# Kernel tuning notes

Measured on AMD Instinct MI355X. Metric: run time of the kernel, lower is better.

## Reference

```python
import jax, jax.numpy as jnp
import numpy as np
import math

B, L, E, H, NL, M, S, R = 4, 1024, 512, 8, 2, 2048, 256, 2
Dh = E // H
NEG = jnp.finfo(jnp.float32).min


def _posenc(n, d):
    pos = np.arange(n)[:, None].astype(np.float32)
    div = np.exp(np.arange(0, d, 2).astype(np.float32) * (-math.log(10000.0) / d))
    pe = np.zeros((n, d), np.float32)
    pe[:, 0::2] = np.sin(pos * div)
    pe[:, 1::2] = np.cos(pos * div)
    return jnp.asarray(pe)


def _temb(t, dim, max_positions=10000):
    half = dim // 2
    freqs = jnp.exp(jnp.arange(half, dtype=jnp.float32) * (-math.log(max_positions) / (half - 1)))
    a = t[:, None] * freqs[None, :]
    return jnp.concatenate([jnp.sin(a), jnp.cos(a)], axis=1)


def _ln(x, s, b, eps=1e-5):
    m = x.mean(-1, keepdims=True)
    v = jnp.mean((x - m) ** 2, axis=-1, keepdims=True)
    return (x - m) * jax.lax.rsqrt(v + eps) * s + b


def _gelu(x):
    return jax.nn.gelu(x, approximate=False)


def _block(h, W, b, lns, lnb, mW1, mb1, mW2, mb2, mask):
    # prenorm self-attention
    z = _ln(h, lns[0], lnb[0])
    q = (z @ W[0] + b[0]).reshape(B, L, H, Dh) / math.sqrt(Dh)
    k = (z @ W[1] + b[1]).reshape(B, L, H, Dh)
    v = (z @ W[2] + b[2]).reshape(B, L, H, Dh)
    logits = jnp.einsum('bqhd,bkhd->bhqk', q, k)
    att = jax.nn.softmax(jnp.where(mask, logits, NEG), axis=-1)
    o = jnp.einsum('bhqk,bkhd->bqhd', att, v).reshape(B, L, E)
    h = h + o @ W[3] + b[3]
    # prenorm feed-forward
    z = _ln(h, lns[1], lnb[1])
    return h + _gelu(z @ mW1 + mb1) @ mW2 + mb2


def setup_inputs():
    key = jax.random.key(0)
    ks = iter(jax.random.split(key, 48))
    def nrm(shape, s=0.02):
        return jax.random.normal(next(ks), shape, jnp.float32) * s
    inp = {
        'x': jax.random.randint(next(ks), (B, L), 0, S),
        't': jax.random.uniform(next(ks), (B,), jnp.float32) * 1000.0,
        'embed': nrm((S, E), 1.0),
        'attn_W': nrm((2, NL, 4, E, E)),
        'attn_b': jnp.zeros((2, NL, 4, E)),
        'ln_s': jnp.ones((2, NL, 2, E)),
        'ln_b': jnp.zeros((2, NL, 2, E)),
        'mlp_W1': nrm((2, NL, E, M)),
        'mlp_b1': jnp.zeros((2, NL, M)),
        'mlp_W2': nrm((2, NL, M, E)),
        'mlp_b2': jnp.zeros((2, NL, E)),
        'ca_Wq': nrm((E, E)),
        'ca_Wk': nrm((E, E)), 'ca_bk': jnp.zeros((E,)),
        'ca_Wv': nrm((E, E)), 'ca_bv': jnp.zeros((E,)),
        'ca_Wo': nrm((E, E)), 'ca_bo': jnp.zeros((E,)),
        'ro_ln1_s': jnp.ones((E,)), 'ro_ln1_b': jnp.zeros((E,)),
        'ro_ln2_s': jnp.ones((E,)), 'ro_ln2_b': jnp.zeros((E,)),
        'in_W': nrm((E, 2 * E)), 'in_b': jnp.zeros((2 * E,)),
        'tmlp_W1': nrm((E, M)), 'tmlp_b1': jnp.zeros((M,)),
        'tmlp_W2': nrm((M, 4 * E)), 'tmlp_b2': jnp.zeros((4 * E,)),
        'res_W1': nrm((R, 2 * E, M)), 'res_b1': jnp.zeros((R, M)),
        'res_W2': nrm((R, M, 2 * E)), 'res_b2': jnp.zeros((R, 2 * E)),
        'res_ln_s': jnp.ones((R, 2 * E)), 'res_ln_b': jnp.zeros((R, 2 * E)),
        'film_W': nrm((R, 4 * E, 4 * E)), 'film_b': jnp.ones((R, 4 * E)),
        'out_W': nrm((2 * E, S)), 'out_b': jnp.zeros((S,)),
    }
    return inp


def reference(x, t, embed, attn_W, attn_b, ln_s, ln_b, mlp_W1, mlp_b1, mlp_W2, mlp_b2,
              ca_Wq, ca_Wk, ca_bk, ca_Wv, ca_bv, ca_Wo, ca_bo,
              ro_ln1_s, ro_ln1_b, ro_ln2_s, ro_ln2_b,
              in_W, in_b, tmlp_W1, tmlp_b1, tmlp_W2, tmlp_b2,
              res_W1, res_b1, res_W2, res_b2, res_ln_s, res_ln_b,
              film_W, film_b, out_W, out_b):
    temb = _temb(t, E)                       # [B,E]
    tok = embed[x]                           # [B,L,E]
    pe = _posenc(L, E)[None]
    cond = temb[:, None, :]
    il = jnp.arange(L)
    causal = (il[None, :] <= il[:, None])[None, None]  # [1,1,L,L]
    embeds = []
    for d in range(2):
        if d == 0:  # l2r: shift right, prepend temb token, causal mask
            h = jnp.concatenate([cond, tok[:, :-1]], axis=1)
            mask = causal
        else:       # r2l: shift left, append temb token, anti-causal mask
            h = jnp.concatenate([tok[:, 1:], cond], axis=1)
            mask = jnp.swapaxes(causal, -1, -2)
        h = h + pe
        for l in range(NL):
            h = _block(h, attn_W[d, l], attn_b[d, l], ln_s[d, l], ln_b[d, l],
                       mlp_W1[d, l], mlp_b1[d, l], mlp_W2[d, l], mlp_b2[d, l], mask)
        embeds.append(h)
    l2r_embed, r2l_embed = embeds
    # AttentionReadout (prenorm) with joint-mask cross-attention
    inputs = l2r_embed + r2l_embed
    l2r_n = _ln(l2r_embed, ro_ln1_s, ro_ln1_b)
    r2l_n = _ln(r2l_embed, ro_ln2_s, ro_ln2_b)
    q = ((l2r_n + r2l_n) @ ca_Wq).reshape(B, L, H, Dh) / math.sqrt(Dh)
    allv = jnp.concatenate([temb[:, None], l2r_n, r2l_n], axis=1)  # [B,2L+1,E]
    k = (allv @ ca_Wk + ca_bk).reshape(B, 2 * L + 1, H, Dh)
    v = (allv @ ca_Wv + ca_bv).reshape(B, 2 * L + 1, H, Dh)
    logits = jnp.einsum('bqhd,bkhd->bhqk', q, k)  # [B,H,L,2L+1]
    m_l2r = il[None, :] > il[:, None]   # triu, diag=1
    m_r2l = il[None, :] < il[:, None]   # tril, diag=-1
    joint = jnp.concatenate([jnp.ones((L, 1), bool), m_l2r, m_r2l], axis=-1)[None, None]
    att = jax.nn.softmax(jnp.where(joint, logits, NEG), axis=-1)
    xat = jnp.einsum('bhqk,bkhd->bqhd', att, v).reshape(B, L, E)
    xat = xat @ ca_Wo + ca_bo + inputs
    # ResidualReadout: FiLM-conditioned residual MLP stack
    t4 = _gelu(temb @ tmlp_W1 + tmlp_b1) @ tmlp_W2 + tmlp_b2  # [B,4E]
    h = xat @ in_W + in_b                                     # [B,L,2E]
    for i in range(R):
        film = t4 @ film_W[i] + film_b[i]
        z = _gelu(h @ res_W1[i] + res_b1[i]) @ res_W2[i] + res_b2[i]
        h = _ln(h + z, res_ln_s[i], res_ln_b[i])
        fa, fb = jnp.split(film[:, None, :], 2, axis=-1)
        h = fa * h + fb
    return h @ out_W + out_b  # [B,L,S]
```

## Files before the change

### kernel.cpp

```cpp
#include <hip/hip_runtime.h>
#include <hip/hip_bf16.h>


#define NEGF -3.4028235e38f
#define LOG2E 1.4426950408889634f

using bf16x8 = __attribute__((ext_vector_type(8))) short;
using f32x4  = __attribute__((ext_vector_type(4))) float;

__device__ inline float bf2f(unsigned short u) {
    return __uint_as_float(((unsigned int)u) << 16);
}
__device__ inline unsigned short f2b(float f) {
    unsigned int u = __float_as_uint(f);
    return (unsigned short)((u + 0x7fff + ((u >> 16) & 1)) >> 16);
}

__device__ inline void gl_lds16(const void* g, void* l) {
    __builtin_amdgcn_global_load_lds(
        (const __attribute__((address_space(1))) void*)(uintptr_t)g,
        (__attribute__((address_space(3))) void*)(unsigned int)(uintptr_t)l,
        16, 0, 0);
}

template<int BM>
__global__ __launch_bounds__(256) void gemm_bf16_k(
    const unsigned short* __restrict__ A,
    const unsigned short* __restrict__ Wt0, const unsigned short* __restrict__ Wt1,
    const float* __restrict__ bias0, const float* __restrict__ bias1, int mhalf,
    const float* __restrict__ res,
    float* __restrict__ Cf, unsigned short* __restrict__ Cb,
    unsigned short* __restrict__ CbK, unsigned short* __restrict__ Ct, int ldkv,
    int M, int N, int K, float alpha, int gelu_flag, int qkv)
{
    constexpr int MF  = BM / 32;
    constexpr int NAC = BM * 4 / 256;
    __shared__ unsigned short As[3][BM * 32];
    __shared__ unsigned short Bs[3][4096];
    const int tid  = threadIdx.x;
    const int wid  = tid >> 6;
    const int lane = tid & 63;
    const int wy   = wid >> 1, wx = wid & 1;
    const int koff = lane >> 4, l16 = lane & 15;

    const int flat = blockIdx.y * gridDim.x + blockIdx.x;
    const int cpx  = (gridDim.x * gridDim.y) >> 3;
    const int swz  = (flat & 7) * cpx + (flat >> 3);
    const int m0 = (swz / gridDim.x) * BM, n0 = (swz % gridDim.x) * 128;

    const unsigned short* Wt = (m0 < mhalf) ? Wt0 : Wt1;
    const float* bias = (m0 < mhalf) ? bias0 : bias1;

    const unsigned short* aG[NAC];
    const unsigned short* bG[2];
    #pragma unroll
    for (int i = 0; i < NAC; ++i) {
        int c = tid + i * 256;
        int r = ((c >> 6) << 4) | (c & 15), kk = ((c >> 4) & 3) << 3;
        aG[i] = A + (size_t)(m0 + r) * K + kk;
    }
    #pragma unroll
    for (int i = 0; i < 2; ++i) {
        int c = tid + i * 256;
        int r = ((c >> 6) << 4) | (c & 15), kk = ((c >> 4) & 3) << 3;
        bG[i] = Wt + (size_t)(n0 + r) * K + kk;
    }

    f32x4 acc[MF][4] = {};
    const int nk = K >> 5;

    auto stage = [&](int buf, int k0) {
        #pragma unroll
        for (int i = 0; i < NAC; ++i)
            gl_lds16(aG[i] + k0, &As[buf][(size_t)(i * 256 + wid * 64) * 8]);
        #pragma unroll
        for (int i = 0; i < 2; ++i)
            gl_lds16(bG[i] + k0, &Bs[buf][(size_t)(i * 256 + wid * 64) * 8]);
    };

    stage(0, 0);
    if (nk > 1) stage(1, 32);
    int cur = 0, nxt = 2;
    for (int it = 0; it < nk; ++it) {
        const int ahead = nk - 1 - it;
        if (ahead >= 2) stage(nxt, (it + 2) << 5);
        if constexpr (BM == 128) {
            if (ahead >= 2)      asm volatile("s_waitcnt vmcnt(8)" ::: "memory");
            else if (ahead == 1) asm volatile("s_waitcnt vmcnt(4)" ::: "memory");
            else                 asm volatile("s_waitcnt vmcnt(0)" ::: "memory");
        } else {
            if (ahead >= 2)      asm volatile("s_waitcnt vmcnt(6)" ::: "memory");
            else if (ahead == 1) asm volatile("s_waitcnt vmcnt(3)" ::: "memory");
            else                 asm volatile("s_waitcnt vmcnt(0)" ::: "memory");
        }
        __builtin_amdgcn_s_barrier();

        bf16x8 af[MF], bfr[4];
        const int foff = (koff * 16 + l16) * 8;
        #pragma unroll
        for (int i = 0; i < MF; ++i)
            af[i] = *(const bf16x8*)&As[cur][(size_t)((wy * MF + i) * 64) * 8 + foff];
        #pragma unroll
        for (int j = 0; j < 4; ++j)
            bfr[j] = *(const bf16x8*)&Bs[cur][(size_t)((wx * 4 + j) * 64) * 8 + foff];
        #pragma unroll
        for (int i = 0; i < MF; ++i)
            #pragma unroll
            for (int j = 0; j < 4; ++j)
                acc[i][j] = __builtin_amdgcn_mfma_f32_16x16x32_bf16(
                    af[i], bfr[j], acc[i][j], 0, 0, 0);

        cur = (cur == 2) ? 0 : cur + 1;
        nxt = (nxt == 2) ? 0 : nxt + 1;
    }

    #pragma unroll
    for (int i = 0; i < MF; ++i) {
        const int rbase = m0 + wy * (MF * 16) + i * 16 + koff * 4;
        #pragma unroll
        for (int j = 0; j < 4; ++j) {
            const int gn = n0 + wx * 64 + j * 16 + l16;
            const float bs = bias ? bias[gn] : 0.f;
            if (qkv) {
                const int seg = gn >> 9, gnl = gn & 511;
                const float av = (seg == 0) ? 0.125f : 1.0f;
                unsigned short o[4];
                #pragma unroll
                for (int r = 0; r < 4; ++r) o[r] = f2b((acc[i][j][r] + bs) * av);
                if (seg == 0) {
                    #pragma unroll
                    for (int r = 0; r < 4; ++r)
                        Cb[(size_t)(rbase + r) * 512 + gnl] = o[r];
                } else if (seg == 1) {
                    #pragma unroll
                    for (int r = 0; r < 4; ++r)
                        CbK[(size_t)(rbase + r) * 512 + gnl] = o[r];
                } else {
                    const int hh = gnl >> 6, dh = gnl & 63;
                    const int bb = rbase >> 10, l0 = rbase & 1023;
                    *(ushort4*)(Ct + ((size_t)(bb * 8 + hh) * 64 + dh) * 1024 + l0) =
                        make_ushort4(o[0], o[1], o[2], o[3]);
                }
            } else {
                float vr[4];
                #pragma unroll
                for (int r = 0; r < 4; ++r) {
                    float v = (acc[i][j][r] + bs) * alpha;
                    if (gelu_flag) v = 0.5f * v * (1.0f + erff(v * 0.70710678118654752f));
                    const size_t idx = (size_t)(rbase + r) * N + gn;
                    if (res) v += res[idx];
                    if (Cf) Cf[idx] = v;
                    if (Cb) Cb[idx] = f2b(v);
                    vr[r] = v;
                }
                if (Ct) {
                    const int hh = gn >> 6, dh = gn & 63;
                    const int bb = rbase / ldkv;
                    const int l0 = rbase - bb * ldkv;
                    *(ushort4*)(Ct + ((size_t)(bb * 8 + hh) * 64 + dh) * ldkv + l0) =
                        make_ushort4(f2b(vr[0]), f2b(vr[1]), f2b(vr[2]), f2b(vr[3]));
                }
            }
        }
    }
}

__global__ __launch_bounds__(256) void wconv(
    const float* __restrict__ src, unsigned short* __restrict__ dst,
    int K, int N, long sstride, long dstride)
{
    __shared__ float t[64][65];
    const int n0 = blockIdx.x * 64, k0 = blockIdx.y * 64;
    const float* s = src + (size_t)blockIdx.z * sstride;
    unsigned short* d = dst + (size_t)blockIdx.z * dstride;
    const int tid = threadIdx.x;
    #pragma unroll
    for (int i = 0; i < 4; ++i) {
        int lin = i * 1024 + tid * 4;
        int r = lin >> 6, c = lin & 63;
        float4 v = *(const float4*)(s + (size_t)(k0 + r) * N + n0 + c);
        t[r][c] = v.x; t[r][c + 1] = v.y; t[r][c + 2] = v.z; t[r][c + 3] = v.w;
    }
    __syncthreads();
    #pragma unroll
    for (int i = 0; i < 8; ++i) {
        int lin = i * 512 + tid * 2;
        int rn = lin >> 6, ck = lin & 63;
        ushort2 o;
        o.x = f2b(t[ck][rn]); o.y = f2b(t[ck + 1][rn]);
        *(ushort2*)(d + (size_t)(n0 + rn) * K + k0 + ck) = o;
    }
}

__global__ __launch_bounds__(256) void skinny_k(
    const float* __restrict__ A, const float* __restrict__ W,
    float* __restrict__ P, int N, int K)
{
    const int n = blockIdx.x * 256 + threadIdx.x;
    const int s = blockIdx.y;
    const int k0 = s * 32;
    float a0 = 0.f, a1 = 0.f, a2 = 0.f, a3 = 0.f;
    #pragma unroll 8
    for (int k = k0; k < k0 + 32; ++k) {
        float w = W[(size_t)k * N + n];
        a0 = fmaf(A[k], w, a0);
        a1 = fmaf(A[K + k], w, a1);
        a2 = fmaf(A[2 * K + k], w, a2);
        a3 = fmaf(A[3 * K + k], w, a3);
    }
    float* p = P + (size_t)s * 4 * N;
    p[n] = a0; p[N + n] = a1; p[2 * N + n] = a2; p[3 * N + n] = a3;
}

__global__ __launch_bounds__(256) void skinny_red(
    const float* __restrict__ P, const float* __restrict__ bias,
    float* __restrict__ C, int N, int nsplit, int gelu_flag)
{
    const int n = blockIdx.x * 256 + threadIdx.x;
    const int r = blockIdx.y;
    float acc = 0.f;
    for (int s = 0; s < nsplit; ++s) acc += P[((size_t)s * 4 + r) * N + n];
    float v = acc + (bias ? bias[n] : 0.f);
    if (gelu_flag) v = 0.5f * v * (1.0f + erff(v * 0.70710678118654752f));
    C[(size_t)r * N + n] = v;
}

__global__ __launch_bounds__(256) void ln_kernel(
    const float* __restrict__ X, const float* __restrict__ X2,
    const float* __restrict__ s, const float* __restrict__ b,
    float* __restrict__ Yf, unsigned short* __restrict__ Yb,
    int D, const float* __restrict__ film, int rows_per_batch, long pstride)
{
    const int row = blockIdx.x;
    const int tid = threadIdx.x;
    const float* x = X + (size_t)row * D;
    const float* x2 = X2 ? X2 + (size_t)row * D : nullptr;
    const float* se = s + (size_t)(row >> 12) * pstride;
    const float* be = b + (size_t)(row >> 12) * pstride;

    float sum = 0.f, sq = 0.f;
    for (int c = tid * 2; c < D; c += 512) {
        float2 v2 = *(const float2*)(x + c);
        if (x2) { float2 w2 = *(const float2*)(x2 + c); v2.x += w2.x; v2.y += w2.y; }
        sum += v2.x + v2.y;
        sq  += v2.x * v2.x + v2.y * v2.y;
    }
    __shared__ float r1[4], r2[4];
    __shared__ float s_mean, s_rstd;
    for (int off = 32; off > 0; off >>= 1) {
        sum += __shfl_down(sum, off);
        sq  += __shfl_down(sq,  off);
    }
    if ((tid & 63) == 0) { r1[tid >> 6] = sum; r2[tid >> 6] = sq; }
    __syncthreads();
    if (tid == 0) {
        float ts = r1[0] + r1[1] + r1[2] + r1[3];
        float tq = r2[0] + r2[1] + r2[2] + r2[3];
        float mean = ts / (float)D;
        float var = tq / (float)D - mean * mean;
        s_mean = mean;
        s_rstd = rsqrtf(var + 1e-5f);
    }
    __syncthreads();
    const float mean = s_mean, rstd = s_rstd;
    const float* fa = nullptr; const float* fb = nullptr;
    if (film) {
        int batch = row / rows_per_batch;
        fa = film + (size_t)batch * 2 * D;
        fb = fa + D;
    }
    for (int c = tid * 2; c < D; c += 512) {
        float2 v2 = *(const float2*)(x + c);
        if (x2) { float2 w2 = *(const float2*)(x2 + c); v2.x += w2.x; v2.y += w2.y; }
        float y0 = (v2.x - mean) * rstd * se[c] + be[c];
        float y1 = (v2.y - mean) * rstd * se[c + 1] + be[c + 1];
        if (film) { y0 = fa[c] * y0 + fb[c]; y1 = fa[c + 1] * y1 + fb[c + 1]; }
        if (Yf) *(float2*)(Yf + (size_t)row * D + c) = make_float2(y0, y1);
        if (Yb) *(ushort2*)(Yb + (size_t)row * D + c) = make_ushort2(f2b(y0), f2b(y1));
    }
}

__global__ __launch_bounds__(256) void readout_fuse(
    const float* __restrict__ L2R, const float* __restrict__ R2L,
    const float* __restrict__ s1, const float* __restrict__ b1,
    const float* __restrict__ s2, const float* __restrict__ b2,
    const unsigned short* __restrict__ tembb,
    float* __restrict__ Z, unsigned short* __restrict__ allv,
    unsigned short* __restrict__ SUM)
{
    const int row = blockIdx.x;
    const int tid = threadIdx.x;
    if (row >= 4096) {
        const int b = row - 4096;
        if (tid < 64)
            ((uint4*)(allv + (size_t)b * 2080 * 512))[tid] =
                ((const uint4*)(tembb + b * 512))[tid];
        return;
    }
    const int b = row >> 10, i = row & 1023;
    const float* x1 = L2R + (size_t)row * 512;
    const float* x2 = R2L + (size_t)row * 512;
    const int c = tid * 2;
    float2 a1 = *(const float2*)(x1 + c);
    float2 a2 = *(const float2*)(x2 + c);

    float su1 = a1.x + a1.y, sk1 = a1.x * a1.x + a1.y * a1.y;
    float su2 = a2.x + a2.y, sk2 = a2.x * a2.x + a2.y * a2.y;
    __shared__ float rr[4][4];
    __shared__ float st[4];
    for (int off = 32; off > 0; off >>= 1) {
        su1 += __shfl_down(su1, off);
        sk1 += __shfl_down(sk1, off);
        su2 += __shfl_down(su2, off);
        sk2 += __shfl_down(sk2, off);
    }
    if ((tid & 63) == 0) {
        rr[tid >> 6][0] = su1; rr[tid >> 6][1] = sk1;
        rr[tid >> 6][2] = su2; rr[tid >> 6][3] = sk2;
    }
    __syncthreads();
    if (tid == 0) {
        float t0 = rr[0][0] + rr[1][0] + rr[2][0] + rr[3][0];
        float t1 = rr[0][1] + rr[1][1] + rr[2][1] + rr[3][1];
        float t2 = rr[0][2] + rr[1][2] + rr[2][2] + rr[3][2];
        float t3 = rr[0][3] + rr[1][3] + rr[2][3] + rr[3][3];
        float m1 = t0 / 512.f, m2 = t2 / 512.f;
        st[0] = m1;
        st[1] = rsqrtf(t1 / 512.f - m1 * m1 + 1e-5f);
        st[2] = m2;
        st[3] = rsqrtf(t3 / 512.f - m2 * m2 + 1e-5f);
    }
    __syncthreads();
    const float m1 = st[0], r1v = st[1], m2 = st[2], r2v = st[3];

    *(float2*)(Z + (size_t)row * 512 + c) = make_float2(a1.x + a2.x, a1.y + a2.y);

    float n1x = (a1.x - m1) * r1v * s1[c]     + b1[c];
    float n1y = (a1.y - m1) * r1v * s1[c + 1] + b1[c + 1];
    float n2x = (a2.x - m2) * r2v * s2[c]     + b2[c];
    float n2y = (a2.y - m2) * r2v * s2[c + 1] + b2[c + 1];

    unsigned short* l2rn = allv + ((size_t)(b * 2080 + 1 + i)) * 512;
    unsigned short* r2ln = allv + ((size_t)(b * 2080 + 1025 + i)) * 512;
    *(ushort2*)(l2rn + c) = make_ushort2(f2b(n1x), f2b(n1y));
    *(ushort2*)(r2ln + c) = make_ushort2(f2b(n2x), f2b(n2y));
    *(ushort2*)(SUM + (size_t)row * 512 + c) =
        make_ushort2(f2b(n1x + n2x), f2b(n1y + n2y));
}

__global__ void temb_kernel(const float* __restrict__ t, float* __restrict__ temb,
                            unsigned short* __restrict__ tembb)
{
    int b = blockIdx.x;
    int i = threadIdx.x;
    float f = expf((float)i * (-9.210340371976184f / 255.0f));
    float a = t[b] * f;
    float sv = sinf(a), cv = cosf(a);
    temb[b * 512 + i]        = sv;
    temb[b * 512 + 256 + i]  = cv;
    tembb[b * 512 + i]       = f2b(sv);
    tembb[b * 512 + 256 + i] = f2b(cv);
}

__global__ void embed_kernel(const int* __restrict__ x, const float* __restrict__ temb,
                             const float* __restrict__ embed,
                             float* __restrict__ l2r, float* __restrict__ r2l)
{
    const int i = blockIdx.x;
    const int b = blockIdx.y;
    const int d = blockIdx.z;
    float* out = (d == 0 ? l2r : r2l) + ((size_t)(b * 1024 + i) * 512);
    const float* src;
    if (d == 0) src = (i == 0)    ? temb + b * 512 : embed + (size_t)x[b * 1024 + (i - 1)] * 512;
    else        src = (i == 1023) ? temb + b * 512 : embed + (size_t)x[b * 1024 + (i + 1)] * 512;
    for (int e = threadIdx.x; e < 512; e += 256) {
        int j = e >> 1;
        float div = expf((float)(2 * j) * (-9.210340371976184f / 512.0f));
        float ang = (float)i * div;
        float pe = (e & 1) ? cosf(ang) : sinf(ang);
        out[e] = src[e] + pe;
    }
}

__global__ __launch_bounds__(256) void attn_mfma(
    const unsigned short* __restrict__ Q, const unsigned short* __restrict__ K,
    const unsigned short* __restrict__ Vt, unsigned short* __restrict__ O, int mode)
{
    const int E = 512;
    const int LKP = (mode == 2) ? 2080 : 1024;
    const int idf = blockIdx.x;
    const int chunk = gridDim.x >> 3;
    const int w = (idf & 7) * chunk + (idf >> 3);
    int h, bb, dir, qn, qtA;
    if (mode == 2) { qn = 1; qtA = w & 15; h = (w >> 4) & 7; bb = w >> 7; dir = 2; }
    else           { qn = 2; qtA = w & 7;  h = (w >> 3) & 7; bb = w >> 6; dir = bb >> 2; }
    const int tid = threadIdx.x;
    const int wid = tid >> 6, lane = tid & 63;
    const int fr = lane & 15;
    const int fs = lane >> 4;

    __shared__ unsigned short Qs[4096];
    __shared__ unsigned short Ks[4096];
    __shared__ unsigned short Vs[4096];
    __shared__ unsigned short Ps[4][16][72];

    const unsigned short* Kb0 = K + ((size_t)bb * LKP) * E + h * 64;
    const unsigned short* Vb0 = Vt + (size_t)(bb * 8 + h) * 64 * LKP;
    const int sr = tid & 63, sc = tid >> 6;

    uint4 kr0, kr1, vr0, vr1;
#define LOAD_TILE(KT) do {                                                     \
        const unsigned short* Kbase_ = Kb0 + (size_t)((KT) * 64) * E;          \
        const unsigned short* Vbase_ = Vb0 + (KT) * 64;                        \
        kr0 = *(const uint4*)(Kbase_ + (size_t)sr * E + sc * 8);               \
        kr1 = *(const uint4*)(Kbase_ + (size_t)sr * E + (sc + 4) * 8);         \
        vr0 = *(const uint4*)(Vbase_ + (size_t)sr * LKP + sc * 8);             \
        vr1 = *(const uint4*)(Vbase_ + (size_t)sr * LKP + (sc + 4) * 8);       \
    } while (0)

    for (int p = 0; p < qn; ++p) {
        const int qt = (p == 0) ? qtA : (15 - qtA);
        const int q0 = qt * 64;
        const int wq0 = q0 + wid * 16;

        {
            const unsigned short* Qbase = Q + ((size_t)bb * 1024 + q0) * E + h * 64;
            #pragma unroll
            for (int it = 0; it < 2; ++it) {
                int i = tid + it * 256;
                int r = i & 63, c = i >> 6;
                *(uint4*)&Qs[(size_t)(c * 64 + r) * 8] =
                    *(const uint4*)(Qbase + (size_t)r * E + c * 8);
            }
        }
        __syncthreads();
        const bf16x8 aq0 = *(const bf16x8*)&Qs[(size_t)(fs * 64 + wid * 16 + fr) * 8];
        const bf16x8 aq1 = *(const bf16x8*)&Qs[(size_t)((fs + 4) * 64 + wid * 16 + fr) * 8];

        float m_r[4], l_r[4];
        f32x4 o_acc[4] = {};
        #pragma unroll
        for (int r = 0; r < 4; ++r) { m_r[r] = NEGF; l_r[r] = 0.f; }

        int nt, ktA = 1;
        if (dir == 0)      nt = qt + 1;
        else if (dir == 1) nt = 16 - qt;
        else { ktA = (qt >= 1) ? qt : 1; nt = 1 + (qt + 16 - ktA + 1); }
        auto kt_of = [&](int j) -> int {
            if (dir == 0) return j;
            if (dir == 1) return qt + j;
            return (j == 0) ? 0 : (ktA + j - 1);
        };

        LOAD_TILE(kt_of(0));

        for (int j = 0; j < nt; ++j) {
            const int kt = kt_of(j);
            const int k0 = kt * 64;

            asm volatile("s_waitcnt lgkmcnt(0)" ::: "memory");
            __builtin_amdgcn_s_barrier();

            *(uint4*)&Ks[(size_t)(sc * 64 + sr) * 8]       = kr0;
            *(uint4*)&Ks[(size_t)((sc + 4) * 64 + sr) * 8] = kr1;
            *(uint4*)&Vs[(size_t)(sc * 64 + sr) * 8]       = vr0;
            *(uint4*)&Vs[(size_t)((sc + 4) * 64 + sr) * 8] = vr1;
            if (j + 1 < nt) LOAD_TILE(kt_of(j + 1));
            else if (p + 1 < qn) {
                const int qt2 = 15 - qtA;
                const int kt2 = (dir == 0) ? 0 : ((dir == 1) ? qt2 : 0);
                LOAD_TILE(kt2);
            }

            asm volatile("s_waitcnt lgkmcnt(0)" ::: "memory");
            __builtin_amdgcn_s_barrier();

            f32x4 s[4] = {};
            __builtin_amdgcn_s_setprio(1);
            #pragma unroll
            for (int t = 0; t < 4; ++t) {
                bf16x8 bk0 = *(const bf16x8*)&Ks[(size_t)(fs * 64 + t * 16 + fr) * 8];
                bf16x8 bk1 = *(const bf16x8*)&Ks[(size_t)((fs + 4) * 64 + t * 16 + fr) * 8];
                s[t] = __builtin_amdgcn_mfma_f32_16x16x32_bf16(aq0, bk0, s[t], 0, 0, 0);
                s[t] = __builtin_amdgcn_mfma_f32_16x16x32_bf16(aq1, bk1, s[t], 0, 0, 0);
            }
            __builtin_amdgcn_s_setprio(0);

            bool need_mask;
            if (dir != 2) need_mask = (kt == qt);
            else if (kt >= 1 && kt <= 15) need_mask = !((64 * kt - 1) > (q0 + 63));
            else if (kt >= 17)            need_mask = !((64 * kt + 63 - 1025) < q0);
            else                          need_mask = true;
            if (need_mask) {
                #pragma unroll
                for (int t = 0; t < 4; ++t) {
                    #pragma unroll
                    for (int r = 0; r < 4; ++r) {
                        int q = wq0 + fs * 4 + r;
                        int k = k0 + t * 16 + fr;
                        bool valid;
                        if (dir == 0)      valid = (k <= q);
                        else if (dir == 1) valid = (k >= q);
                        else valid = (k == 0) || (k <= 1024 ? (k - 1) > q : (k - 1025) < q);
                        if (!valid) s[t][r] = NEGF;
                    }
                }
            }

            float c_[4], rs[4];
            #pragma unroll
            for (int r = 0; r < 4; ++r) {
                float v = fmaxf(fmaxf(s[0][r], s[1][r]), fmaxf(s[2][r], s[3][r]));
                v = fmaxf(v, __shfl_xor(v, 1));
                v = fmaxf(v, __shfl_xor(v, 2));
                v = fmaxf(v, __shfl_xor(v, 4));
                v = fmaxf(v, __shfl_xor(v, 8));
                float mnew = fmaxf(m_r[r], v);
                c_[r] = exp2f((m_r[r] - mnew) * LOG2E);
                m_r[r] = mnew;
                rs[r] = 0.f;
            }
            #pragma unroll
            for (int t = 0; t < 4; ++t) {
                #pragma unroll
                for (int r = 0; r < 4; ++r) {
                    float pv = exp2f((s[t][r] - m_r[r]) * LOG2E);
                    s[t][r] = pv;
                    rs[r] += pv;
                }
            }
            #pragma unroll
            for (int r = 0; r < 4; ++r) {
                float v = rs[r];
                v += __shfl_xor(v, 1);
                v += __shfl_xor(v, 2);
                v += __shfl_xor(v, 4);
                v += __shfl_xor(v, 8);
                l_r[r] = l_r[r] * c_[r] + v;
                o_acc[0][r] *= c_[r]; o_acc[1][r] *= c_[r];
                o_acc[2][r] *= c_[r]; o_acc[3][r] *= c_[r];
            }

            #pragma unroll
            for (int t = 0; t < 4; ++t)
                #pragma unroll
                for (int r = 0; r < 4; ++r)
                    Ps[wid][fs * 4 + r][t * 16 + fr] = f2b(s[t][r]);

            bf16x8 pa0 = *(const bf16x8*)&Ps[wid][fr][fs * 8];
            bf16x8 pa1 = *(const bf16x8*)&Ps[wid][fr][fs * 8 + 32];
            __builtin_amdgcn_s_setprio(1);
            #pragma unroll
            for (int t = 0; t < 4; ++t) {
                bf16x8 bv0 = *(const bf16x8*)&Vs[(size_t)(fs * 64 + t * 16 + fr) * 8];
                bf16x8 bv1 = *(const bf16x8*)&Vs[(size_t)((fs + 4) * 64 + t * 16 + fr) * 8];
                o_acc[t] = __builtin_amdgcn_mfma_f32_16x16x32_bf16(pa0, bv0, o_acc[t], 0, 0, 0);
                o_acc[t] = __builtin_amdgcn_mfma_f32_16x16x32_bf16(pa1, bv1, o_acc[t], 0, 0, 0);
            }
            __builtin_amdgcn_s_setprio(0);
        }

        unsigned short* Obase = O + ((size_t)bb * 1024 + q0) * E + h * 64;
        float invl[4];
        #pragma unroll
        for (int r = 0; r < 4; ++r) invl[r] = 1.f / l_r[r];
        #pragma unroll
        for (int t = 0; t < 4; ++t)
            #pragma unroll
            for (int r = 0; r < 4; ++r)
                Obase[(size_t)(wid * 16 + fs * 4 + r) * E + t * 16 + fr] =
                    f2b(o_acc[t][r] * invl[r]);

        if (p + 1 < qn) __syncthreads();
    }
#undef LOAD_TILE
}


static inline void gemmb(hipStream_t st, int BM, const unsigned short* A,
                         const unsigned short* Wt0, const unsigned short* Wt1,
                         const float* bias0, const float* bias1, int mhalf,
                         const float* res, float* Cf, unsigned short* Cb,
                         unsigned short* CbK, unsigned short* Ct, int ldkv,
                         int M, int N, int K, float alpha, int gelu, int qkv)
{
    dim3 g(N / 128, M / BM);
    if (BM == 128)
        gemm_bf16_k<128><<<g, dim3(256), 0, st>>>(A, Wt0, Wt1, bias0, bias1, mhalf,
            res, Cf, Cb, CbK, Ct, ldkv, M, N, K, alpha, gelu, qkv);
    else
        gemm_bf16_k<64><<<g, dim3(256), 0, st>>>(A, Wt0, Wt1, bias0, bias1, mhalf,
            res, Cf, Cb, CbK, Ct, ldkv, M, N, K, alpha, gelu, qkv);
}

static inline void sgemm4(hipStream_t st, const float* A, const float* W,
                          const float* bias, float* C, float* P,
                          int N, int K, int gelu)
{
    const int nsplit = K / 32;
    skinny_k<<<dim3(N / 256, nsplit), 256, 0, st>>>(A, W, P, N, K);
    skinny_red<<<dim3(N / 256, 4), 256, 0, st>>>(P, bias, C, N, nsplit, gelu);
}

extern "C" void kernel_launch(void* const* d_in, const int* in_sizes, int n_in,
                              void* d_out, int out_size, void* d_ws, size_t ws_size,
                              hipStream_t stream)
{
    const int*   x      = (const int*)  d_in[0];
    const float* t      = (const float*)d_in[1];
    const float* embedW = (const float*)d_in[2];
    const float* attn_W = (const float*)d_in[3];
    const float* attn_b = (const float*)d_in[4];
    const float* ln_s   = (const float*)d_in[5];
    const float* ln_b   = (const float*)d_in[6];
    const float* mlp_W1 = (const float*)d_in[7];
    const float* mlp_b1 = (const float*)d_in[8];
    const float* mlp_W2 = (const float*)d_in[9];
    const float* mlp_b2 = (const float*)d_in[10];
    const float* ca_Wq  = (const float*)d_in[11];
    const float* ca_Wk  = (const float*)d_in[12];
    const float* ca_bk  = (const float*)d_in[13];
    const float* ca_Wv  = (const float*)d_in[14];
    const float* ca_bv  = (const float*)d_in[15];
    const float* ca_Wo  = (const float*)d_in[16];
    const float* ca_bo  = (const float*)d_in[17];
    const float* ro1s   = (const float*)d_in[18];
    const float* ro1b   = (const float*)d_in[19];
    const float* ro2s   = (const float*)d_in[20];
    const float* ro2b   = (const float*)d_in[21];
    const float* in_W   = (const float*)d_in[22];
    const float* in_b   = (const float*)d_in[23];
    const float* tm_W1  = (const float*)d_in[24];
    const float* tm_b1  = (const float*)d_in[25];
    const float* tm_W2  = (const float*)d_in[26];
    const float* tm_b2  = (const float*)d_in[27];
    const float* res_W1 = (const float*)d_in[28];
    const float* res_b1 = (const float*)d_in[29];
    const float* res_W2 = (const float*)d_in[30];
    const float* res_b2 = (const float*)d_in[31];
    const float* rls    = (const float*)d_in[32];
    const float* rlb    = (const float*)d_in[33];
    const float* film_W = (const float*)d_in[34];
    const float* film_b = (const float*)d_in[35];
    const float* out_W  = (const float*)d_in[36];
    const float* out_b  = (const float*)d_in[37];
    float* out = (float*)d_out;
    (void)ws_size; (void)in_sizes; (void)n_in; (void)out_size;

    char* base = (char*)d_ws;
    size_t off = 0;
    auto alloc = [&](size_t bytes) -> char* {
        char* p = base + off;
        off = (off + bytes + 255) & ~(size_t)255;
        return p;
    };
    float* TEMB  = (float*)alloc(8192);
    float* TM1   = (float*)alloc(32768);
    float* T4    = (float*)alloc(32768);
    float* FILM  = (float*)alloc(32768);
    unsigned short* TEMBb = (unsigned short*)alloc(4096);
    float* SKP   = (float*)alloc(2097152);

    float* HB  = (float*)alloc(16777216);
    float* L2R = HB;
    float* R2L = HB + 4096 * 512;
    float* Z   = (float*)alloc(8388608);
    float* H2  = (float*)alloc(16777216);
    float* Z2  = (float*)alloc(16777216);

    unsigned short* Zb  = (unsigned short*)alloc(8388608);
    unsigned short* Qb  = (unsigned short*)alloc(8388608);
    unsigned short* Kb  = (unsigned short*)alloc(8388608);
    unsigned short* Vb  = (unsigned short*)alloc(8388608);
    unsigned short* Ob  = (unsigned short*)alloc(8388608);
    unsigned short* H2b = (unsigned short*)alloc(8388608);

    unsigned short* BIG = (unsigned short*)alloc(33554432);
    unsigned short* MIDb  = BIG;
    unsigned short* ALLVb = BIG;
    unsigned short* K2b   = BIG + 4259840;
    unsigned short* V2T   = BIG + 8519680;

    unsigned short* WT = (unsigned short*)alloc(45613056);
    const size_t wt_attn = 0,        wt_mlp1 = 4194304, wt_mlp2 = 8388608;
    const size_t wt_caq = 12582912,  wt_cak = 12845056, wt_cav = 13107200,
                 wt_cao = 13369344,  wt_in  = 13631488;
    const size_t wt_res1 = 14155776, wt_res2 = 18350080, wt_out = 22544384;

    wconv<<<dim3(8, 8, 16), 256, 0, stream>>>(attn_W, WT + wt_attn, 512, 512, 262144, 262144);
    wconv<<<dim3(32, 8, 4), 256, 0, stream>>>(mlp_W1, WT + wt_mlp1, 512, 2048, 1048576, 1048576);
    wconv<<<dim3(8, 32, 4), 256, 0, stream>>>(mlp_W2, WT + wt_mlp2, 2048, 512, 1048576, 1048576);
    wconv<<<dim3(8, 8), 256, 0, stream>>>(ca_Wq, WT + wt_caq, 512, 512, 0, 0);
    wconv<<<dim3(8, 8), 256, 0, stream>>>(ca_Wk, WT + wt_cak, 512, 512, 0, 0);
    wconv<<<dim3(8, 8), 256, 0, stream>>>(ca_Wv, WT + wt_cav, 512, 512, 0, 0);
    wconv<<<dim3(8, 8), 256, 0, stream>>>(ca_Wo, WT + wt_cao, 512, 512, 0, 0);
    wconv<<<dim3(16, 8), 256, 0, stream>>>(in_W, WT + wt_in, 512, 1024, 0, 0);
    wconv<<<dim3(32, 16, 2), 256, 0, stream>>>(res_W1, WT + wt_res1, 1024, 2048, 2097152, 2097152);
    wconv<<<dim3(16, 32, 2), 256, 0, stream>>>(res_W2, WT + wt_res2, 2048, 1024, 2097152, 2097152);
    wconv<<<dim3(4, 16), 256, 0, stream>>>(out_W, WT + wt_out, 1024, 256, 0, 0);

    temb_kernel<<<dim3(4), dim3(256), 0, stream>>>(t, TEMB, TEMBb);
    embed_kernel<<<dim3(1024, 4, 2), dim3(256), 0, stream>>>(x, TEMB, embedW, L2R, R2L);

    for (int l = 0; l < 2; ++l) {
        const size_t d1 = 2 + l;
        ln_kernel<<<8192, 256, 0, stream>>>(HB, nullptr,
            ln_s + (l * 2 + 0) * 512, ln_b + (l * 2 + 0) * 512,
            nullptr, Zb, 512, nullptr, 1024, 2048);
        gemmb(stream, 64, Zb,
              WT + wt_attn + (size_t)l * 1048576, WT + wt_attn + d1 * 1048576,
              attn_b + l * 2048, attn_b + d1 * 2048, 4096,
              nullptr, nullptr, Qb, Kb, Vb, 1024, 8192, 1536, 512, 1.f, 0, 1);
        attn_mfma<<<dim3(512), dim3(256), 0, stream>>>(Qb, Kb, Vb, Ob, -1);
        gemmb(stream, 64, Ob,
              WT + wt_attn + (size_t)(l * 4 + 3) * 262144,
              WT + wt_attn + (d1 * 4 + 3) * 262144,
              attn_b + (l * 4 + 3) * 512, attn_b + (d1 * 4 + 3) * 512, 4096,
              HB, HB, nullptr, nullptr, nullptr, 1, 8192, 512, 512, 1.f, 0, 0);
        ln_kernel<<<8192, 256, 0, stream>>>(HB, nullptr,
            ln_s + (l * 2 + 1) * 512, ln_b + (l * 2 + 1) * 512,
            nullptr, Zb, 512, nullptr, 1024, 2048);
        gemmb(stream, 64, Zb,
              WT + wt_mlp1 + (size_t)l * 1048576, WT + wt_mlp1 + d1 * 1048576,
              mlp_b1 + l * 2048, mlp_b1 + d1 * 2048, 4096,
              nullptr, nullptr, MIDb, nullptr, nullptr, 1, 8192, 2048, 512, 1.f, 1, 0);
        gemmb(stream, 64, MIDb,
              WT + wt_mlp2 + (size_t)l * 1048576, WT + wt_mlp2 + d1 * 1048576,
              mlp_b2 + l * 512, mlp_b2 + d1 * 512, 4096,
              HB, HB, nullptr, nullptr, nullptr, 1, 8192, 512, 2048, 1.f, 0, 0);
    }

    readout_fuse<<<dim3(4100), 256, 0, stream>>>(L2R, R2L, ro1s, ro1b, ro2s, ro2b,
                                                 TEMBb, Z, ALLVb, Vb);
    gemmb(stream, 64, Vb, WT + wt_caq, WT + wt_caq, nullptr, nullptr, 1 << 30,
          nullptr, nullptr, Zb, nullptr, nullptr, 1, 4096, 512, 512, 0.125f, 0, 0);
    gemmb(stream, 64, ALLVb, WT + wt_cak, WT + wt_cak, ca_bk, ca_bk, 1 << 30,
          nullptr, nullptr, K2b, nullptr, nullptr, 1, 8320, 512, 512, 1.f, 0, 0);
    gemmb(stream, 64, ALLVb, WT + wt_cav, WT + wt_cav, ca_bv, ca_bv, 1 << 30,
          nullptr, nullptr, nullptr, nullptr, V2T, 2080, 8320, 512, 512, 1.f, 0, 0);
    attn_mfma<<<dim3(512), dim3(256), 0, stream>>>(Zb, K2b, V2T, Ob, 2);
    gemmb(stream, 64, Ob, WT + wt_cao, WT + wt_cao, ca_bo, ca_bo, 1 << 30,
          Z, nullptr, Qb, nullptr, nullptr, 1, 4096, 512, 512, 1.f, 0, 0);

    sgemm4(stream, TEMB, tm_W1, tm_b1, TM1, SKP, 2048, 512, 1);
    sgemm4(stream, TM1, tm_W2, tm_b2, T4, SKP, 2048, 2048, 0);

    gemmb(stream, 64, Qb, WT + wt_in, WT + wt_in, in_b, in_b, 1 << 30,
          nullptr, H2, H2b, nullptr, nullptr, 1, 4096, 1024, 512, 1.f, 0, 0);
    for (int i = 0; i < 2; ++i) {
        sgemm4(stream, T4, film_W + (size_t)i * 4194304, film_b + i * 2048,
               FILM, SKP, 2048, 2048, 0);
        gemmb(stream, 64, H2b, WT + wt_res1 + (size_t)i * 2097152,
              WT + wt_res1 + (size_t)i * 2097152,
              res_b1 + i * 2048, res_b1 + i * 2048, 1 << 30,
              nullptr, nullptr, MIDb, nullptr, nullptr, 1, 4096, 2048, 1024, 1.f, 1, 0);
        gemmb(stream, 64, MIDb, WT + wt_res2 + (size_t)i * 2097152,
              WT + wt_res2 + (size_t)i * 2097152,
              res_b2 + i * 1024, res_b2 + i * 1024, 1 << 30,
              nullptr, Z2, nullptr, nullptr, nullptr, 1, 4096, 1024, 2048, 1.f, 0, 0);
        ln_kernel<<<4096, 256, 0, stream>>>(H2, Z2, rls + i * 1024, rlb + i * 1024,
                                            H2, H2b, 1024, FILM, 1024, 0);
    }

    gemmb(stream, 64, H2b, WT + wt_out, WT + wt_out, out_b, out_b, 1 << 30,
          nullptr, out, nullptr, nullptr, nullptr, 1, 4096, 256, 1024, 1.f, 0, 0);
}
```

Baseline: 1.047 ms.

## Add 256x256-tile 512-thread bf16 GEMM kernel and use it for large GEMMs

Adds a new GEMM kernel with 256x256 output tiles, 512 threads and a triple-buffered global-to-LDS pipeline. It also adds a swizzled block-to-tile mapping and raises wave priority with s_setprio around the MFMA loop. The kernel replaces the 64-row tile kernel for the transformer QKV, out-proj, MLP and readout GEMMs, aiming for more operand reuse per block and fewer global loads. The epilogue is factored into a shared macro. The trade-off is that shapes with small N now launch only 64–256 blocks, which may leave many of the device's CUs idle.

```diff
diff --git a/kernel.cpp b/kernel.cpp
--- a/kernel.cpp
+++ b/kernel.cpp
@@ -22,6 +22,51 @@
         (__attribute__((address_space(3))) void*)(unsigned int)(uintptr_t)l,
         16, 0, 0);
 }
+
+#define GEMM_EPILOGUE(ACC, RBASE, GN)                                          \
+    do {                                                                       \
+        const float bs = bias ? bias[GN] : 0.f;                                \
+        if (qkv) {                                                             \
+            const int seg = (GN) >> 9, gnl = (GN) & 511;                       \
+            const float av = (seg == 0) ? 0.125f : 1.0f;                       \
+            unsigned short o[4];                                               \
+            _Pragma("unroll")                                                  \
+            for (int r = 0; r < 4; ++r) o[r] = f2b(((ACC)[r] + bs) * av);      \
+            if (seg == 0) {                                                    \
+                _Pragma("unroll")                                              \
+                for (int r = 0; r < 4; ++r)                                    \
+                    Cb[(size_t)((RBASE) + r) * 512 + gnl] = o[r];              \
+            } else if (seg == 1) {                                             \
+                _Pragma("unroll")                                              \
+                for (int r = 0; r < 4; ++r)                                    \
+                    CbK[(size_t)((RBASE) + r) * 512 + gnl] = o[r];             \
+            } else {                                                           \
+                const int hh = gnl >> 6, dh = gnl & 63;                        \
+                const int bbx = (RBASE) >> 10, l0 = (RBASE) & 1023;            \
+                *(ushort4*)(Ct + ((size_t)(bbx * 8 + hh) * 64 + dh) * 1024 + l0) = \
+                    make_ushort4(o[0], o[1], o[2], o[3]);                      \
+            }                                                                  \
+        } else {                                                               \
+            float vr[4];                                                       \
+            _Pragma("unroll")                                                  \
+            for (int r = 0; r < 4; ++r) {                                      \
+                float v = ((ACC)[r] + bs) * alpha;                             \
+                if (gelu_flag) v = 0.5f * v * (1.0f + erff(v * 0.70710678118654752f)); \
+                const size_t idx = (size_t)((RBASE) + r) * N + (GN);           \
+                if (res) v += res[idx];                                        \
+                if (Cf) Cf[idx] = v;                                           \
+                if (Cb) Cb[idx] = f2b(v);                                      \
+                vr[r] = v;                                                     \
+            }                                                                  \
+            if (Ct) {                                                          \
+                const int hh = (GN) >> 6, dh = (GN) & 63;                      \
+                const int bbx = (RBASE) / ldkv;                                \
+                const int l0 = (RBASE) - bbx * ldkv;                           \
+                *(ushort4*)(Ct + ((size_t)(bbx * 8 + hh) * 64 + dh) * ldkv + l0) = \
+                    make_ushort4(f2b(vr[0]), f2b(vr[1]), f2b(vr[2]), f2b(vr[3])); \
+            }                                                                  \
+        }                                                                      \
+    } while (0)
 
 template<int BM>
 __global__ __launch_bounds__(256) void gemm_bf16_k(
@@ -120,47 +165,96 @@
         #pragma unroll
         for (int j = 0; j < 4; ++j) {
             const int gn = n0 + wx * 64 + j * 16 + l16;
-            const float bs = bias ? bias[gn] : 0.f;
-            if (qkv) {
-                const int seg = gn >> 9, gnl = gn & 511;
-                const float av = (seg == 0) ? 0.125f : 1.0f;
-                unsigned short o[4];
-                #pragma unroll
-                for (int r = 0; r < 4; ++r) o[r] = f2b((acc[i][j][r] + bs) * av);
-                if (seg == 0) {
-                    #pragma unroll
-                    for (int r = 0; r < 4; ++r)
-                        Cb[(size_t)(rbase + r) * 512 + gnl] = o[r];
-                } else if (seg == 1) {
-                    #pragma unroll
-                    for (int r = 0; r < 4; ++r)
-                        CbK[(size_t)(rbase + r) * 512 + gnl] = o[r];
-                } else {
-                    const int hh = gnl >> 6, dh = gnl & 63;
-                    const int bb = rbase >> 10, l0 = rbase & 1023;
-                    *(ushort4*)(Ct + ((size_t)(bb * 8 + hh) * 64 + dh) * 1024 + l0) =
-                        make_ushort4(o[0], o[1], o[2], o[3]);
-                }
-            } else {
-                float vr[4];
-                #pragma unroll
-                for (int r = 0; r < 4; ++r) {
-                    float v = (acc[i][j][r] + bs) * alpha;
-                    if (gelu_flag) v = 0.5f * v * (1.0f + erff(v * 0.70710678118654752f));
-                    const size_t idx = (size_t)(rbase + r) * N + gn;
-                    if (res) v += res[idx];
-                    if (Cf) Cf[idx] = v;
-                    if (Cb) Cb[idx] = f2b(v);
-                    vr[r] = v;
-                }
-                if (Ct) {
-                    const int hh = gn >> 6, dh = gn & 63;
-                    const int bb = rbase / ldkv;
-                    const int l0 = rbase - bb * ldkv;
-                    *(ushort4*)(Ct + ((size_t)(bb * 8 + hh) * 64 + dh) * ldkv + l0) =
-                        make_ushort4(f2b(vr[0]), f2b(vr[1]), f2b(vr[2]), f2b(vr[3]));
-                }
-            }
+            GEMM_EPILOGUE(acc[i][j], rbase, gn);
+        }
+    }
+}
+
+__global__ __launch_bounds__(512) void gemm_bf16_256(
+    const unsigned short* __restrict__ A,
+    const unsigned short* __restrict__ Wt0, const unsigned short* __restrict__ Wt1,
+    const float* __restrict__ bias0, const float* __restrict__ bias1, int mhalf,
+    const float* __restrict__ res,
+    float* __restrict__ Cf, unsigned short* __restrict__ Cb,
+    unsigned short* __restrict__ CbK, unsigned short* __restrict__ Ct, int ldkv,
+    int M, int N, int K, float alpha, int gelu_flag, int qkv)
+{
+    __shared__ unsigned short As[3][256 * 32];
+    __shared__ unsigned short Bs[3][256 * 32];
+    const int tid  = threadIdx.x;
+    const int wid  = tid >> 6;
+    const int lane = tid & 63;
+    const int wy   = wid >> 2, wx = wid & 3;
+    const int koff = lane >> 4, l16 = lane & 15;
+
+    const int flat = blockIdx.y * gridDim.x + blockIdx.x;
+    const int cpx  = (gridDim.x * gridDim.y) >> 3;
+    const int swz  = (flat & 7) * cpx + (flat >> 3);
+    const int m0 = (swz / gridDim.x) * 256, n0 = (swz % gridDim.x) * 256;
+
+    const unsigned short* Wt = (m0 < mhalf) ? Wt0 : Wt1;
+    const float* bias = (m0 < mhalf) ? bias0 : bias1;
+
+    const unsigned short* aG[2];
+    const unsigned short* bG[2];
+    #pragma unroll
+    for (int i = 0; i < 2; ++i) {
+        int c = tid + i * 512;
+        int r = ((c >> 6) << 4) | (c & 15), kk = ((c >> 4) & 3) << 3;
+        aG[i] = A + (size_t)(m0 + r) * K + kk;
+        bG[i] = Wt + (size_t)(n0 + r) * K + kk;
+    }
+
+    f32x4 acc[8][4] = {};
+    const int nk = K >> 5;
+
+    auto stage = [&](int buf, int k0) {
+        #pragma unroll
+        for (int i = 0; i < 2; ++i)
+            gl_lds16(aG[i] + k0, &As[buf][(size_t)(i * 512 + wid * 64) * 8]);
+        #pragma unroll
+        for (int i = 0; i < 2; ++i)
+            gl_lds16(bG[i] + k0, &Bs[buf][(size_t)(i * 512 + wid * 64) * 8]);
+    };
+
+    stage(0, 0);
+    if (nk > 1) stage(1, 32);
+    int cur = 0, nxt = 2;
+    for (int it = 0; it < nk; ++it) {
+        const int ahead = nk - 1 - it;
+        if (ahead >= 2) stage(nxt, (it + 2) << 5);
+        if (ahead >= 2)      asm volatile("s_waitcnt vmcnt(8)" ::: "memory");
+        else if (ahead == 1) asm volatile("s_waitcnt vmcnt(4)" ::: "memory");
+        else                 asm volatile("s_waitcnt vmcnt(0)" ::: "memory");
+        __builtin_amdgcn_s_barrier();
+
+        const int foff = (koff * 16 + l16) * 8;
+        bf16x8 bfr[4];
+        #pragma unroll
+        for (int j = 0; j < 4; ++j)
+            bfr[j] = *(const bf16x8*)&Bs[cur][(size_t)((wx * 4 + j) * 64) * 8 + foff];
+        __builtin_amdgcn_s_setprio(1);
+        #pragma unroll
+        for (int i = 0; i < 8; ++i) {
+            bf16x8 af = *(const bf16x8*)&As[cur][(size_t)((wy * 8 + i) * 64) * 8 + foff];
+            #pragma unroll
+            for (int j = 0; j < 4; ++j)
+                acc[i][j] = __builtin_amdgcn_mfma_f32_16x16x32_bf16(
+                    af, bfr[j], acc[i][j], 0, 0, 0);
+        }
+        __builtin_amdgcn_s_setprio(0);
+
+        cur = (cur == 2) ? 0 : cur + 1;
+        nxt = (nxt == 2) ? 0 : nxt + 1;
+    }
+
+    #pragma unroll
+    for (int i = 0; i < 8; ++i) {
+        const int rbase = m0 + wy * 128 + i * 16 + koff * 4;
+        #pragma unroll
+        for (int j = 0; j < 4; ++j) {
+            const int gn = n0 + wx * 64 + j * 16 + l16;
+            GEMM_EPILOGUE(acc[i][j], rbase, gn);
         }
     }
 }
@@ -584,13 +678,19 @@
                          unsigned short* CbK, unsigned short* Ct, int ldkv,
                          int M, int N, int K, float alpha, int gelu, int qkv)
 {
-    dim3 g(N / 128, M / BM);
-    if (BM == 128)
+    if (BM == 256) {
+        dim3 g(N / 256, M / 256);
+        gemm_bf16_256<<<g, dim3(512), 0, st>>>(A, Wt0, Wt1, bias0, bias1, mhalf,
+            res, Cf, Cb, CbK, Ct, ldkv, M, N, K, alpha, gelu, qkv);
+    } else if (BM == 128) {
+        dim3 g(N / 128, M / 128);
         gemm_bf16_k<128><<<g, dim3(256), 0, st>>>(A, Wt0, Wt1, bias0, bias1, mhalf,
             res, Cf, Cb, CbK, Ct, ldkv, M, N, K, alpha, gelu, qkv);
-    else
+    } else {
+        dim3 g(N / 128, M / 64);
         gemm_bf16_k<64><<<g, dim3(256), 0, st>>>(A, Wt0, Wt1, bias0, bias1, mhalf,
             res, Cf, Cb, CbK, Ct, ldkv, M, N, K, alpha, gelu, qkv);
+    }
 }
 
 static inline void sgemm4(hipStream_t st, const float* A, const float* W,
@@ -707,12 +807,12 @@
         ln_kernel<<<8192, 256, 0, stream>>>(HB, nullptr,
             ln_s + (l * 2 + 0) * 512, ln_b + (l * 2 + 0) * 512,
             nullptr, Zb, 512, nullptr, 1024, 2048);
-        gemmb(stream, 64, Zb,
+        gemmb(stream, 256, Zb,
               WT + wt_attn + (size_t)l * 1048576, WT + wt_attn + d1 * 1048576,
               attn_b + l * 2048, attn_b + d1 * 2048, 4096,
               nullptr, nullptr, Qb, Kb, Vb, 1024, 8192, 1536, 512, 1.f, 0, 1);
         attn_mfma<<<dim3(512), dim3(256), 0, stream>>>(Qb, Kb, Vb, Ob, -1);
-        gemmb(stream, 64, Ob,
+        gemmb(stream, 256, Ob,
               WT + wt_attn + (size_t)(l * 4 + 3) * 262144,
               WT + wt_attn + (d1 * 4 + 3) * 262144,
               attn_b + (l * 4 + 3) * 512, attn_b + (d1 * 4 + 3) * 512, 4096,
@@ -720,11 +820,11 @@
         ln_kernel<<<8192, 256, 0, stream>>>(HB, nullptr,
             ln_s + (l * 2 + 1) * 512, ln_b + (l * 2 + 1) * 512,
             nullptr, Zb, 512, nullptr, 1024, 2048);
-        gemmb(stream, 64, Zb,
+        gemmb(stream, 256, Zb,
               WT + wt_mlp1 + (size_t)l * 1048576, WT + wt_mlp1 + d1 * 1048576,
               mlp_b1 + l * 2048, mlp_b1 + d1 * 2048, 4096,
               nullptr, nullptr, MIDb, nullptr, nullptr, 1, 8192, 2048, 512, 1.f, 1, 0);
-        gemmb(stream, 64, MIDb,
+        gemmb(stream, 256, MIDb,
               WT + wt_mlp2 + (size_t)l * 1048576, WT + wt_mlp2 + d1 * 1048576,
               mlp_b2 + l * 512, mlp_b2 + d1 * 512, 4096,
               HB, HB, nullptr, nullptr, nullptr, 1, 8192, 512, 2048, 1.f, 0, 0);
@@ -745,16 +845,16 @@
     sgemm4(stream, TEMB, tm_W1, tm_b1, TM1, SKP, 2048, 512, 1);
     sgemm4(stream, TM1, tm_W2, tm_b2, T4, SKP, 2048, 2048, 0);
 
-    gemmb(stream, 64, Qb, WT + wt_in, WT + wt_in, in_b, in_b, 1 << 30,
+    gemmb(stream, 256, Qb, WT + wt_in, WT + wt_in, in_b, in_b, 1 << 30,
           nullptr, H2, H2b, nullptr, nullptr, 1, 4096, 1024, 512, 1.f, 0, 0);
     for (int i = 0; i < 2; ++i) {
         sgemm4(stream, T4, film_W + (size_t)i * 4194304, film_b + i * 2048,
                FILM, SKP, 2048, 2048, 0);
-        gemmb(stream, 64, H2b, WT + wt_res1 + (size_t)i * 2097152,
+        gemmb(stream, 256, H2b, WT + wt_res1 + (size_t)i * 2097152,
               WT + wt_res1 + (size_t)i * 2097152,
               res_b1 + i * 2048, res_b1 + i * 2048, 1 << 30,
               nullptr, nullptr, MIDb, nullptr, nullptr, 1, 4096, 2048, 1024, 1.f, 1, 0);
-        gemmb(stream, 64, MIDb, WT + wt_res2 + (size_t)i * 2097152,
+        gemmb(stream, 256, MIDb, WT + wt_res2 + (size_t)i * 2097152,
               WT + wt_res2 + (size_t)i * 2097152,
               res_b2 + i * 1024, res_b2 + i * 1024, 1 << 30,
               nullptr, Z2, nullptr, nullptr, nullptr, 1, 4096, 1024, 2048, 1.f, 0, 0);
```

After: 1.758 ms. 1.68x slower.
